# Kernel optimization log

Hardware: AMD Instinct MI355X
Metric: run time of the kernel (lower is better)

The kernel has to match this reference:

```python
import jax, jax.numpy as jnp
import numpy as np

CNN_DIM = 256
CLASS_NUM = 6
NHOPS = 2
ATT_DIM = 50


def conv1d(x, w, b, pad):
    # x: [B, Cin, L], w: [Cout, Cin, K]
    y = jax.lax.conv_general_dilated(x, w, (1,), [(pad, pad)],
                                     dimension_numbers=('NCH', 'OIH', 'NCH'))
    return y + b[None, :, None]


def setup_inputs() -> dict:
    key = jax.random.key(0)
    ks = jax.random.split(key, 16)
    B, L, V, GE, DE = 8, 128, 30000, 300, 100
    IN = GE + DE
    C = CLASS_NUM
    s = 0.02
    inp = {}
    inp['x'] = jax.random.randint(ks[0], (B, L), 0, V)
    inp['x_len'] = L  # python int, stands in for x_len[0] (max length)
    inp['x_mask'] = jnp.ones((B, L), dtype=jnp.float32)
    inp['gen_table'] = jax.random.normal(ks[1], (V, GE), jnp.float32) * s
    inp['domain_table'] = jax.random.normal(ks[2], (V, DE), jnp.float32) * s
    inp['w1'] = jax.random.normal(ks[3], (128, IN, 5)) * s
    inp['b1'] = jnp.zeros((128,))
    inp['w2'] = jax.random.normal(ks[4], (128, IN, 3)) * s
    inp['b2'] = jnp.zeros((128,))
    inp['w3'] = jax.random.normal(ks[5], (256, 256, 5)) * s
    inp['b3'] = jnp.zeros((256,))
    inp['w4'] = jax.random.normal(ks[6], (256, 256, 5)) * s
    inp['b4'] = jnp.zeros((256,))
    inp['w5'] = jax.random.normal(ks[7], (256, 256, 5)) * s
    inp['b5'] = jnp.zeros((256,))
    inp['wq'] = jax.random.normal(ks[8], (CNN_DIM, ATT_DIM)) * s
    inp['bq'] = jnp.zeros((ATT_DIM,))
    inp['wv'] = jax.random.normal(ks[9], (CNN_DIM, ATT_DIM)) * s
    inp['bv'] = jnp.zeros((ATT_DIM,))
    inp['vv'] = jax.random.normal(ks[10], (ATT_DIM,)) * s
    inp['wf'] = jax.random.normal(ks[11], (2 * CNN_DIM + 3 * C, 2 * CNN_DIM)) * s
    inp['bf'] = jnp.zeros((2 * CNN_DIM,))
    inp['wc'] = jax.random.normal(ks[12], (2 * CNN_DIM, C)) * s
    inp['bc'] = jnp.zeros((C,))
    return inp


def reference(x, x_len, x_mask, gen_table, domain_table,
              w1, b1, w2, b2, w3, b3, w4, b4, w5, b5,
              wq, bq, wv, bv, vv, wf, bf, wc, bc):
    # embeddings (dropout omitted: eval mode)
    emb = jnp.concatenate([gen_table[x], domain_table[x]], axis=2)  # [B,L,400]
    xe = jnp.swapaxes(emb, 1, 2)  # [B,400,L]
    xc = jax.nn.relu(jnp.concatenate([conv1d(xe, w1, b1, 2),
                                      conv1d(xe, w2, b2, 1)], axis=1))
    xc = jax.nn.relu(conv1d(xc, w3, b3, 2))
    xc = jax.nn.relu(conv1d(xc, w4, b4, 2))
    xc = jax.nn.relu(conv1d(xc, w5, b5, 2))
    xc = jnp.swapaxes(xc, 1, 2)[:, :x_len, :]  # [B,L,256]
    mask = x_mask[:, :x_len]
    # perceptron (additive) self-attention: v^T tanh(Wq q_i + Wv v_j)
    q = xc @ wq + bq  # [B,L,50]
    v = xc @ wv + bv  # [B,L,50]
    scores = jnp.tanh(q[:, :, None, :] + v[:, None, :, :]) @ vv  # [B,L,L]
    scores = jnp.where(mask[:, None, :] == 0, -1e9, scores)
    attn = jax.nn.softmax(scores, axis=2)
    merged = jnp.einsum('bij,bjd->bid', attn, xc) * mask[:, :, None]
    xc = xc + merged
    B, L, D = xc.shape
    # grid features: (i,j) -> [h_i, h_j]
    features = jnp.concatenate([
        jnp.broadcast_to(xc[:, :, None, :], (B, L, L, D)),
        jnp.broadcast_to(xc[:, None, :, :], (B, L, L, D))], axis=3)  # [B,L,L,512]
    # upper-triangular validity mask on the grid
    m2 = jnp.triu(mask[:, None, :] * mask[:, :, None])[..., None]  # [B,L,L,1]
    logits = features @ wc + bc  # [B,L,L,C]
    for _ in range(NHOPS):
        probs = logits
        lg = probs * m2
        lm = jnp.maximum(jnp.max(lg, axis=1), jnp.max(lg, axis=2))  # [B,L,C]
        row = jnp.broadcast_to(lm[:, :, None, :], (B, L, L, lm.shape[-1]))
        grid = jnp.concatenate([row, jnp.swapaxes(row, 1, 2)], axis=3)  # [B,L,L,2C]
        features = jnp.concatenate([features, grid, probs], axis=3) @ wf + bf
        logits = features @ wc + bc
    return logits
```

## Files before the change

### kernel.cpp

```cpp
#include <hip/hip_runtime.h>
#include <math.h>

#define LSEQ 128
#define BB 8
#define M_TOK (BB*LSEQ)

typedef __attribute__((ext_vector_type(8))) short short8;
typedef __attribute__((ext_vector_type(4))) float floatx4;

__device__ __forceinline__ unsigned short bf16_rne(float v) {
    union { float f; unsigned u; } a; a.f = v;
    return (unsigned short)((a.u + 0x7fffu + ((a.u >> 16) & 1u)) >> 16);
}
__device__ __forceinline__ float bf16_to_f(unsigned short h) {
    union { unsigned u; float f; } b; b.u = ((unsigned)h) << 16;
    return b.f;
}
__device__ __forceinline__ void split2(float v, unsigned short& h, unsigned short& l) {
    h = bf16_rne(v);
    l = bf16_rne(v - bf16_to_f(h));
}

struct PreArgs {
    const float *w1, *w2, *w3, *w4, *w5;
    unsigned short *B1h, *B1l, *B2h, *B2l, *B3h, *B3l, *B4h, *B4l, *B5h, *B5l;
    const int* x;
    const float* gen;
    const float* dom;
    unsigned short *Eh, *El;
    const float* wf;
    const float* wc;
    float* Wfc;
};
__global__ __launch_bounds__(256) void stage_kernel(PreArgs a) {
    int y = blockIdx.y;
    int tid = threadIdx.x;
    if (y < 3) {
        const float* w = (y == 0) ? a.w3 : (y == 1) ? a.w4 : a.w5;
        unsigned short* dh = (y == 0) ? a.B3h : (y == 1) ? a.B4h : a.B5h;
        unsigned short* dl = (y == 0) ? a.B3l : (y == 1) ? a.B4l : a.B5l;
        int idx = blockIdx.x * 256 + tid;
        int j = idx & 7;
        int n = (idx >> 3) & 255;
        int g = idx >> 11;
        int cg = g & 31, kk = g >> 5;
        int ci = cg * 8 + j;
        float v = w[(n * 256 + ci) * 5 + kk];
        unsigned short h, l; split2(v, h, l);
        dh[idx] = h; dl[idx] = l;
    } else if (y == 3) {
        int idx = blockIdx.x * 256 + tid;
        if (idx >= 5 * 52 * 128 * 8) return;
        int j = idx & 7;
        int n = (idx >> 3) & 127;
        int g = idx >> 10;
        int cg = g % 52, kk = g / 52;
        int ci = cg * 8 + j;
        float v = (ci < 400) ? a.w1[(n * 400 + ci) * 5 + kk] : 0.f;
        unsigned short h, l; split2(v, h, l);
        a.B1h[idx] = h; a.B1l[idx] = l;
    } else if (y == 4) {
        int idx = blockIdx.x * 256 + tid;
        if (idx >= 3 * 52 * 128 * 8) return;
        int j = idx & 7;
        int n = (idx >> 3) & 127;
        int g = idx >> 10;
        int cg = g % 52, kk = g / 52;
        int ci = cg * 8 + j;
        float v = (ci < 400) ? a.w2[(n * 400 + ci) * 3 + kk] : 0.f;
        unsigned short h, l; split2(v, h, l);
        a.B2h[idx] = h; a.B2l[idx] = l;
    } else if (y == 5) {
        int m = blockIdx.x;
        if (m >= M_TOK) return;
        int t = a.x[m];
        for (int c = tid; c < 416; c += 256) {
            float v = (c < 300) ? a.gen[t * 300 + c]
                    : (c < 400) ? a.dom[t * 100 + (c - 300)] : 0.f;
            unsigned short h, l; split2(v, h, l);
            a.Eh[m * 416 + c] = h;
            a.El[m * 416 + c] = l;
        }
    } else {
        int r = blockIdx.x;
        if (r >= 512 || tid >= 64) return;
        int l = tid;
        float p[6] = {0,0,0,0,0,0};
        const float* row = a.wf + r * 512;
        #pragma unroll
        for (int k = 0; k < 8; ++k) {
            int n = l + 64 * k;
            float v = row[n];
            #pragma unroll
            for (int c = 0; c < 6; ++c) p[c] += v * a.wc[n * 6 + c];
        }
        #pragma unroll
        for (int c = 0; c < 6; ++c)
            for (int off = 32; off >= 1; off >>= 1) p[c] += __shfl_xor(p[c], off, 64);
        if (l == 0) {
            #pragma unroll
            for (int c = 0; c < 6; ++c) a.Wfc[r * 6 + c] = p[c];
        }
    }
}

__global__ __launch_bounds__(256) void conv1_mfma(
        const unsigned short* __restrict__ Eh, const unsigned short* __restrict__ El,
        const unsigned short* __restrict__ B1h, const unsigned short* __restrict__ B1l,
        const unsigned short* __restrict__ B2h, const unsigned short* __restrict__ B2l,
        const float* __restrict__ b1, const float* __restrict__ b2,
        unsigned short* __restrict__ Xoh, unsigned short* __restrict__ Xol,
        const float* __restrict__ wf, const float* __restrict__ bf,
        const float* __restrict__ wc, const float* __restrict__ Wfc,
        float* __restrict__ U) {
    __shared__ __align__(16) unsigned short xsh[20 * 424];
    __shared__ __align__(16) unsigned short xsl[20 * 424];
    int by = blockIdx.y;
    int tid = threadIdx.x;
    if (by == 4) {
        if (tid >= 64) return;
        int l = tid;
        for (int i = 0; i < 9; ++i) {
            int r = blockIdx.x + 64 * i;
            if (r >= 531) break;
            const float* row = (r < 530) ? (wf + r * 512) : bf;
            float p[12];
            #pragma unroll
            for (int c = 0; c < 12; ++c) p[c] = 0.f;
            #pragma unroll
            for (int k = 0; k < 8; ++k) {
                int n = l + 64 * k;
                float v = row[n];
                #pragma unroll
                for (int c = 0; c < 6; ++c) {
                    p[c]     += v * wc[n * 6 + c];
                    p[c + 6] += v * Wfc[n * 6 + c];
                }
            }
            #pragma unroll
            for (int c = 0; c < 12; ++c)
                for (int off = 32; off >= 1; off >>= 1) p[c] += __shfl_xor(p[c], off, 64);
            if (l == 0) {
                #pragma unroll
                for (int c = 0; c < 12; ++c) U[r * 12 + c] = p[c];
            }
        }
        return;
    }
    int mt = blockIdx.x;
    int p0 = mt * 16;
    int b = p0 >> 7, l0 = p0 & 127;
    for (int i = tid; i < 2 * 1040; i += 256) {
        int sel = i >= 1040;
        int u2 = sel ? i - 1040 : i;
        int j = u2 / 52, cg = u2 % 52;
        int l = l0 - 2 + j;
        short8 v = {0,0,0,0,0,0,0,0};
        if (l >= 0 && l < 128) {
            const unsigned short* src = (sel ? El : Eh) + (b * 128 + l) * 416 + cg * 8;
            v = *(const short8*)src;
        }
        *(short8*)((sel ? xsl : xsh) + j * 424 + cg * 8) = v;
    }
    __syncthreads();
    int w = tid >> 6, lane = tid & 63;
    int m = lane & 15, q = lane >> 4;
    bool br2 = (by >= 2);
    int n0b = (by & 1) * 64;
    int nB = n0b + w * 16 + m;
    floatx4 acc0 = {0,0,0,0}, acc1 = {0,0,0,0}, acc2 = {0,0,0,0};
    if (!br2) {
        for (int kk = 0; kk < 5; ++kk) {
            const unsigned short* arh = xsh + (m + kk) * 424;
            const unsigned short* arl = xsl + (m + kk) * 424;
            #pragma unroll
            for (int u = 0; u < 13; ++u) {
                short8 ah = *(const short8*)(arh + u * 32 + q * 8);
                short8 al = *(const short8*)(arl + u * 32 + q * 8);
                int boff = (((kk * 52 + u * 4 + q) * 128) + nB) * 8;
                short8 bh = *(const short8*)(B1h + boff);
                short8 bl = *(const short8*)(B1l + boff);
                acc0 = __builtin_amdgcn_mfma_f32_16x16x32_bf16(ah, bh, acc0, 0, 0, 0);
                acc1 = __builtin_amdgcn_mfma_f32_16x16x32_bf16(ah, bl, acc1, 0, 0, 0);
                acc2 = __builtin_amdgcn_mfma_f32_16x16x32_bf16(al, bh, acc2, 0, 0, 0);
            }
        }
    } else {
        for (int kk = 0; kk < 3; ++kk) {
            const unsigned short* arh = xsh + (m + kk + 1) * 424;
            const unsigned short* arl = xsl + (m + kk + 1) * 424;
            #pragma unroll
            for (int u = 0; u < 13; ++u) {
                short8 ah = *(const short8*)(arh + u * 32 + q * 8);
                short8 al = *(const short8*)(arl + u * 32 + q * 8);
                int boff = (((kk * 52 + u * 4 + q) * 128) + nB) * 8;
                short8 bh = *(const short8*)(B2h + boff);
                short8 bl = *(const short8*)(B2l + boff);
                acc0 = __builtin_amdgcn_mfma_f32_16x16x32_bf16(ah, bh, acc0, 0, 0, 0);
                acc1 = __builtin_amdgcn_mfma_f32_16x16x32_bf16(ah, bl, acc1, 0, 0, 0);
                acc2 = __builtin_amdgcn_mfma_f32_16x16x32_bf16(al, bh, acc2, 0, 0, 0);
            }
        }
    }
    __syncthreads();
    float* fl = (float*)xsh;
    #pragma unroll
    for (int reg = 0; reg < 4; ++reg)
        fl[(q * 4 + reg) * 68 + w * 16 + m] = acc0[reg] + acc1[reg] + acc2[reg];
    __syncthreads();
    int ocb = br2 ? 128 + n0b : n0b;
    const float* bias = br2 ? b2 : b1;
    #pragma unroll
    for (int i = 0; i < 4; ++i) {
        int e = tid + 256 * i;
        int mm = e >> 6, nn = e & 63;
        float val = fl[mm * 68 + nn] + bias[n0b + nn];
        val = fmaxf(val, 0.f);
        unsigned short h, l; split2(val, h, l);
        int o = (p0 + mm) * 256 + ocb + nn;
        Xoh[o] = h; Xol[o] = l;
    }
}

__global__ __launch_bounds__(256) void conv256_mfma(
        const unsigned short* __restrict__ Xih, const unsigned short* __restrict__ Xil,
        const unsigned short* __restrict__ Bh, const unsigned short* __restrict__ Bl,
        const float* __restrict__ bias, int outmode,
        unsigned short* __restrict__ Xoh, unsigned short* __restrict__ Xol,
        float* __restrict__ fout) {
    __shared__ __align__(16) unsigned short xsh[20 * 264];
    __shared__ __align__(16) unsigned short xsl[20 * 264];
    int mt = blockIdx.x;
    int p0 = mt * 16;
    int b = p0 >> 7, l0 = p0 & 127;
    int n0 = blockIdx.y * 64;
    int tid = threadIdx.x;
    for (int i = tid; i < 2 * 640; i += 256) {
        int sel = i >= 640;
        int u2 = sel ? i - 640 : i;
        int j = u2 >> 5, cg = u2 & 31;
        int l = l0 - 2 + j;
        short8 v = {0,0,0,0,0,0,0,0};
        if (l >= 0 && l < 128) {
            const unsigned short* src = (sel ? Xil : Xih) + (b * 128 + l) * 256 + cg * 8;
            v = *(const short8*)src;
        }
        *(short8*)((sel ? xsl : xsh) + j * 264 + cg * 8) = v;
    }
    __syncthreads();
    int w = tid >> 6, lane = tid & 63;
    int m = lane & 15, q = lane >> 4;
    int nB = n0 + w * 16 + m;
    floatx4 acc0 = {0,0,0,0}, acc1 = {0,0,0,0}, acc2 = {0,0,0,0};
    for (int kk = 0; kk < 5; ++kk) {
        const unsigned short* arh = xsh + (m + kk) * 264;
        const unsigned short* arl = xsl + (m + kk) * 264;
        #pragma unroll
        for (int u = 0; u < 8; ++u) {
            short8 ah = *(const short8*)(arh + u * 32 + q * 8);
            short8 al = *(const short8*)(arl + u * 32 + q * 8);
            int boff = (((kk * 32 + u * 4 + q) * 256) + nB) * 8;
            short8 bh = *(const short8*)(Bh + boff);
            short8 bl = *(const short8*)(Bl + boff);
            acc0 = __builtin_amdgcn_mfma_f32_16x16x32_bf16(ah, bh, acc0, 0, 0, 0);
        acc1 = __builtin_amdgcn_mfma_f32_16x16x32_bf16(ah, bl, acc1, 0, 0, 0);
            acc2 = __builtin_amdgcn_mfma_f32_16x16x32_bf16(al, bh, acc2, 0, 0, 0);
        }
    }
    __syncthreads();
    float* fl = (float*)xsh;
    #pragma unroll
    for (int reg = 0; reg < 4; ++reg)
        fl[(q * 4 + reg) * 68 + w * 16 + m] = acc0[reg] + acc1[reg] + acc2[reg];
    __syncthreads();
    #pragma unroll
    for (int i = 0; i < 4; ++i) {
        int e = tid + 256 * i;
        int mm = e >> 6, nn = e & 63;
        float val = fl[mm * 68 + nn] + bias[n0 + nn];
        val = fmaxf(val, 0.f);
        int o = (p0 + mm) * 256 + n0 + nn;
        if (outmode == 0) {
            unsigned short h, l; split2(val, h, l);
            Xoh[o] = h; Xol[o] = l;
        } else {
            fout[o] = val;
        }
    }
}

__global__ __launch_bounds__(128) void qv_v2(const float* __restrict__ xc,
        const float* __restrict__ wq, const float* __restrict__ bq,
        const float* __restrict__ wv, const float* __restrict__ bv,
        float* __restrict__ q, float* __restrict__ v) {
    int m = blockIdx.x;
    int tid = threadIdx.x;
    int w = tid >> 6, d = tid & 63;
    if (d >= 50) return;
    const float* W = w ? wv : wq;
    float a = w ? bv[d] : bq[d];
    const float* xm = xc + m * 256;
    #pragma unroll 8
    for (int c = 0; c < 256; ++c) a += xm[c] * W[c * 50 + d];
    (w ? v : q)[m * 50 + d] = a;
}

__global__ __launch_bounds__(256) void attn_v2(const float* __restrict__ xc,
        const float* __restrict__ q, const float* __restrict__ v,
        const float* __restrict__ vv, const float* __restrict__ xmask,
        const float* __restrict__ wc, const float* __restrict__ bc,
        float* __restrict__ xc2, float* __restrict__ f0, float* __restrict__ g0) {
    __shared__ float vs[128 * 50];
    __shared__ float spart[128], aarr[128], xrow[256], qrow[52], vvs[52], red[4];
    int bi = blockIdx.x;
    int b = bi >> 7;
    int tid = threadIdx.x;
    for (int idx = tid; idx < 128 * 50; idx += 256) vs[idx] = v[b * 6400 + idx];
    if (tid < 50) { qrow[tid] = q[bi * 50 + tid]; vvs[tid] = vv[tid]; }
    __syncthreads();
    int j = tid & 127, half = tid >> 7;
    int d0 = half * 25;
    const float* vj = vs + j * 50 + d0;
    float s = 0.f;
    #pragma unroll
    for (int d = 0; d < 25; ++d) {
        float x = qrow[d0 + d] + vj[d];
        float e = __expf(2.f * x);
        s += (1.f - 2.f / (e + 1.f)) * vvs[d0 + d];
    }
    if (half) spart[j] = s;
    __syncthreads();
    float stot = 0.f;
    if (!half) {
        stot = s + spart[j];
        if (xmask[b * LSEQ + j] == 0.f) stot = -1e9f;
    }
    if (tid < 128) {
        float m = stot;
        #pragma unroll
        for (int off = 32; off >= 1; off >>= 1) m = fmaxf(m, __shfl_xor(m, off, 64));
        if ((tid & 63) == 0) red[tid >> 6] = m;
    }
    __syncthreads();
    float mx = fmaxf(red[0], red[1]);
    float e = 0.f;
    if (tid < 128) {
        e = __expf(stot - mx);
        float su = e;
        #pragma unroll
        for (int off = 32; off >= 1; off >>= 1) su += __shfl_xor(su, off, 64);
        if ((tid & 63) == 0) red[2 + (tid >> 6)] = su;
    }
    __syncthreads();
    float denom = red[2] + red[3];
    if (tid < 128) aarr[j] = e / denom;
    __syncthreads();
    float maskI = xmask[bi];
    const float* xcb = xc + b * LSEQ * 256;
    float acc = 0.f;
    #pragma unroll 8
    for (int jj = 0; jj < 128; ++jj) acc += aarr[jj] * xcb[jj * 256 + tid];
    float val = xc[bi * 256 + tid] + acc * maskI;
    xc2[bi * 256 + tid] = val;
    xrow[tid] = val;
    __syncthreads();
    int grp = tid >> 4, l16 = tid & 15;
    if (grp < 12) {
        int c = grp % 6, gsel = grp / 6;
        const float* wcc = wc + gsel * 256 * 6 + c;
        float a = 0.f;
        #pragma unroll
        for (int ch = l16; ch < 256; ch += 16) a += xrow[ch] * wcc[ch * 6];
        #pragma unroll
        for (int off = 8; off >= 1; off >>= 1) a += __shfl_down(a, off, 16);
        if (l16 == 0) {
            if (gsel == 0) f0[bi * 6 + c] = a + bc[c];
            else           g0[bi * 6 + c] = a;
        }
    }
}

__global__ __launch_bounds__(128) void lm_scan_v3(const float* __restrict__ f,
        const float* __restrict__ g, int stride, float* __restrict__ lm) {
    __shared__ float sf[128], sg[128];
    int bc = blockIdx.x;
    int b = bc / 6, c = bc - b * 6;
    int p = threadIdx.x;
    float fv = f[(b * LSEQ + p) * stride + c];
    float gv = g[(b * LSEQ + p) * stride + c];
    sf[p] = fv; sg[p] = gv;
    __syncthreads();
    float pf = fv, sgx = gv;
    #pragma unroll
    for (int off = 1; off < 128; off <<= 1) {
        float a = (p >= off) ? sf[p - off] : -INFINITY;
        float d = (p + off < 128) ? sg[p + off] : -INFINITY;
        __syncthreads();
        pf = fmaxf(pf, a); sgx = fmaxf(sgx, d);
        sf[p] = pf; sg[p] = sgx;
        __syncthreads();
    }
    float M1 = pf + gv;
    if (p < LSEQ - 1) M1 = fmaxf(M1, 0.f);
    float M2 = fv + sgx;
    if (p > 0) M2 = fmaxf(M2, 0.f);
    lm[(b * LSEQ + p) * 6 + c] = fmaxf(M1, M2);
}

__global__ __launch_bounds__(64) void hopfold_kernel(const float* __restrict__ xc2,
        const float* __restrict__ U, const float* __restrict__ lm0,
        const float* __restrict__ f0, const float* __restrict__ g0,
        const float* __restrict__ bc,
        float* __restrict__ outF, float* __restrict__ outG) {
    int m = blockIdx.x;
    int y = blockIdx.y;
    int tid = threadIdx.x;
    const float* Urows = U + (y ? 256 : 0) * 12;
    float p[12];
    #pragma unroll
    for (int c = 0; c < 12; ++c) p[c] = 0.f;
    for (int k = tid; k < 256; k += 64) {
        float a = xc2[m * 256 + k];
        const float* ur = Urows + k * 12;
        #pragma unroll
        for (int c = 0; c < 12; ++c) p[c] += a * ur[c];
    }
    #pragma unroll
    for (int c = 0; c < 12; ++c)
        for (int off = 32; off >= 1; off >>= 1) p[c] += __shfl_xor(p[c], off, 64);
    if (tid == 0) {
        const float* Bb = U + (y ? 518 : 512) * 12;
        const float* Db = U + 524 * 12;
        const float* fg = y ? g0 : f0;
        float* out = y ? outG : outF;
        float lmv[6], fgv[6];
        #pragma unroll
        for (int j = 0; j < 6; ++j) { lmv[j] = lm0[m * 6 + j]; fgv[j] = fg[m * 6 + j]; }
        #pragma unroll
        for (int c = 0; c < 12; ++c) {
            float s = p[c];
            #pragma unroll
            for (int j = 0; j < 6; ++j) s += lmv[j] * Bb[j * 12 + c] + fgv[j] * Db[j * 12 + c];
            if (!y) { s += U[530 * 12 + c]; if (c < 6) s += bc[c]; }
            out[m * 12 + c] = s;
        }
    }
}

__global__ __launch_bounds__(128) void f2g2_kernel(const float* __restrict__ f1phi,
        const float* __restrict__ g1gam, const float* __restrict__ lm1,
        const float* __restrict__ U, const float* __restrict__ bc,
        float* __restrict__ f2, float* __restrict__ g2) {
    __shared__ float Us[19 * 12], bcs[6];
    int tid = threadIdx.x;
    for (int i = tid; i < 19 * 12; i += 128) Us[i] = U[512 * 12 + i];
    if (tid < 6) bcs[tid] = bc[tid];
    __syncthreads();
    int m = blockIdx.x * 128 + tid;
    float lmv[6], f1v[6], g1v[6];
    #pragma unroll
    for (int j = 0; j < 6; ++j) {
        lmv[j] = lm1[m * 6 + j];
        f1v[j] = f1phi[m * 12 + j];
        g1v[j] = g1gam[m * 12 + j];
    }
    #pragma unroll
    for (int c = 0; c < 6; ++c) {
        float sf = f1phi[m * 12 + 6 + c] + Us[18 * 12 + c] + bcs[c];
        float sg = g1gam[m * 12 + 6 + c];
        #pragma unroll
        for (int j = 0; j < 6; ++j) {
            sf += lmv[j] * Us[j * 12 + c]       + f1v[j] * Us[(12 + j) * 12 + c];
            sg += lmv[j] * Us[(6 + j) * 12 + c] + g1v[j] * Us[(12 + j) * 12 + c];
        }
        f2[m * 6 + c] = sf;
        g2[m * 6 + c] = sg;
    }
}

__global__ __launch_bounds__(256) void writeout_kernel(const float* __restrict__ f2,
        const float* __restrict__ g2, float* __restrict__ out) {
    int idx = blockIdx.x * 256 + threadIdx.x;
    int c = idx % 6;
    int r = idx / 6;
    int j = r & 127;
    int bi = r >> 7;
    int b = bi >> 7;
    out[idx] = f2[bi * 6 + c] + g2[(b * LSEQ + j) * 6 + c];
}

extern "C" void kernel_launch(void* const* d_in, const int* in_sizes, int n_in,
                              void* d_out, int out_size, void* d_ws, size_t ws_size,
                              hipStream_t stream) {
    const int*   x     = (const int*)d_in[0];
    const float* xmask = (const float*)d_in[2];
    const float* gen   = (const float*)d_in[3];
    const float* dom   = (const float*)d_in[4];
    const float* w1    = (const float*)d_in[5];
    const float* b1    = (const float*)d_in[6];
    const float* w2    = (const float*)d_in[7];
    const float* b2    = (const float*)d_in[8];
    const float* w3    = (const float*)d_in[9];
    const float* b3    = (const float*)d_in[10];
    const float* w4    = (const float*)d_in[11];
    const float* b4    = (const float*)d_in[12];
    const float* w5    = (const float*)d_in[13];
    const float* b5    = (const float*)d_in[14];
    const float* wq    = (const float*)d_in[15];
    const float* bq    = (const float*)d_in[16];
    const float* wv    = (const float*)d_in[17];
    const float* bv    = (const float*)d_in[18];
    const float* vv    = (const float*)d_in[19];
    const float* wf    = (const float*)d_in[20];
    const float* bf    = (const float*)d_in[21];
    const float* wc    = (const float*)d_in[22];
    const float* bc    = (const float*)d_in[23];

    float* fb = (float*)d_ws;
    float* bufB  = fb;
    float* xc2   = bufB  + 262144;
    float* qb    = xc2   + 262144;
    float* vb    = qb    + 51200;
    float* Wfc   = vb    + 51200;
    float* U     = Wfc   + 3072;
    float* f0    = U     + 6376;
    float* g0    = f0    + 6144;
    float* lm0   = g0    + 6144;
    float* lm1   = lm0   + 6144;
    float* f1phi = lm1   + 6144;
    float* g1gam = f1phi + 12288;
    float* f2    = g1gam + 12288;
    float* g2    = f2    + 6144;
    unsigned short* sb = (unsigned short*)(g2 + 6144 + 32);
    unsigned short* Eh  = sb;             sb += 425984;
    unsigned short* El  = sb;             sb += 425984;
    unsigned short* B1h = sb;             sb += 266240;
    unsigned short* B1l = sb;             sb += 266240;
    unsigned short* B2h = sb;             sb += 159744;
    unsigned short* B2l = sb;             sb += 159744;
    unsigned short* B3h = sb;             sb += 327680;
    unsigned short* B3l = sb;             sb += 327680;
    unsigned short* B4h = sb;             sb += 327680;
    unsigned short* B4l = sb;             sb += 327680;
    unsigned short* B5h = sb;             sb += 327680;
    unsigned short* B5l = sb;             sb += 327680;
    unsigned short* X3h = sb;             sb += 262144;
    unsigned short* X3l = sb;             sb += 262144;
    unsigned short* X4h = sb;             sb += 262144;
    unsigned short* X4l = sb;             sb += 262144;

    PreArgs pa;
    pa.w1 = w1; pa.w2 = w2; pa.w3 = w3; pa.w4 = w4; pa.w5 = w5;
    pa.B1h = B1h; pa.B1l = B1l; pa.B2h = B2h; pa.B2l = B2l;
    pa.B3h = B3h; pa.B3l = B3l; pa.B4h = B4h; pa.B4l = B4l;
    pa.B5h = B5h; pa.B5l = B5l;
    pa.x = x; pa.gen = gen; pa.dom = dom; pa.Eh = Eh; pa.El = El;
    pa.wf = wf; pa.wc = wc; pa.Wfc = Wfc;
    stage_kernel<<<dim3(1280, 7), 256, 0, stream>>>(pa);

    conv1_mfma<<<dim3(64, 5), 256, 0, stream>>>(Eh, El, B1h, B1l, B2h, B2l, b1, b2,
                                                X3h, X3l, wf, bf, wc, Wfc, U);
    conv256_mfma<<<dim3(64, 4), 256, 0, stream>>>(X3h, X3l, B3h, B3l, b3, 0,
                                                  X4h, X4l, nullptr);
    conv256_mfma<<<dim3(64, 4), 256, 0, stream>>>(X4h, X4l, B4h, B4l, b4, 0,
                                                  X3h, X3l, nullptr);
    conv256_mfma<<<dim3(64, 4), 256, 0, stream>>>(X3h, X3l, B5h, B5l, b5, 1,
                                                  nullptr, nullptr, bufB);

    qv_v2<<<M_TOK, 128, 0, stream>>>(bufB, wq, bq, wv, bv, qb, vb);
    attn_v2<<<M_TOK, 256, 0, stream>>>(bufB, qb, vb, vv, xmask, wc, bc, xc2, f0, g0);

    lm_scan_v3<<<48, 128, 0, stream>>>(f0, g0, 6, lm0);
    hopfold_kernel<<<dim3(M_TOK, 2), 64, 0, stream>>>(xc2, U, lm0, f0, g0, bc, f1phi, g1gam);
    lm_scan_v3<<<48, 128, 0, stream>>>(f1phi, g1gam, 12, lm1);
    f2g2_kernel<<<8, 128, 0, stream>>>(f1phi, g1gam, lm1, U, bc, f2, g2);

    writeout_kernel<<<(BB*LSEQ*LSEQ*6)/256, 256, 0, stream>>>(f2, g2, (float*)d_out);
}
```

Before: 241.0 us.

## Fuse lm max-scans into hop kernels and merge final tail into one kernel

Removes the two separate lm_scan launches by computing the prefix and suffix maxima inside hopfold (a wave-wide masked reduction per token) and inside a new tail kernel (a warp shuffle scan over a shared-memory transposed tile). The f2/g2 computation and the full-grid writeout are merged into tail2_kernel, so the intermediate f2/g2 buffers are no longer written and re-read. This cuts the launch count from five to two and drops the small serial kernels. In exchange, every block redundantly recomputes the per-batch scans and reloads the per-batch f/g data.

```diff
diff --git a/kernel.cpp b/kernel.cpp
--- a/kernel.cpp
+++ b/kernel.cpp
@@ -263,7 +263,7 @@
             short8 bh = *(const short8*)(Bh + boff);
             short8 bl = *(const short8*)(Bl + boff);
             acc0 = __builtin_amdgcn_mfma_f32_16x16x32_bf16(ah, bh, acc0, 0, 0, 0);
-        acc1 = __builtin_amdgcn_mfma_f32_16x16x32_bf16(ah, bl, acc1, 0, 0, 0);
+            acc1 = __builtin_amdgcn_mfma_f32_16x16x32_bf16(ah, bl, acc1, 0, 0, 0);
             acc2 = __builtin_amdgcn_mfma_f32_16x16x32_bf16(al, bh, acc2, 0, 0, 0);
         }
     }
@@ -380,65 +380,68 @@
     }
 }
 
-__global__ __launch_bounds__(128) void lm_scan_v3(const float* __restrict__ f,
-        const float* __restrict__ g, int stride, float* __restrict__ lm) {
-    __shared__ float sf[128], sg[128];
-    int bc = blockIdx.x;
-    int b = bc / 6, c = bc - b * 6;
-    int p = threadIdx.x;
-    float fv = f[(b * LSEQ + p) * stride + c];
-    float gv = g[(b * LSEQ + p) * stride + c];
-    sf[p] = fv; sg[p] = gv;
-    __syncthreads();
-    float pf = fv, sgx = gv;
-    #pragma unroll
-    for (int off = 1; off < 128; off <<= 1) {
-        float a = (p >= off) ? sf[p - off] : -INFINITY;
-        float d = (p + off < 128) ? sg[p + off] : -INFINITY;
-        __syncthreads();
-        pf = fmaxf(pf, a); sgx = fmaxf(sgx, d);
-        sf[p] = pf; sg[p] = sgx;
-        __syncthreads();
-    }
-    float M1 = pf + gv;
-    if (p < LSEQ - 1) M1 = fmaxf(M1, 0.f);
-    float M2 = fv + sgx;
-    if (p > 0) M2 = fmaxf(M2, 0.f);
-    lm[(b * LSEQ + p) * 6 + c] = fmaxf(M1, M2);
-}
-
-__global__ __launch_bounds__(64) void hopfold_kernel(const float* __restrict__ xc2,
-        const float* __restrict__ U, const float* __restrict__ lm0,
-        const float* __restrict__ f0, const float* __restrict__ g0,
-        const float* __restrict__ bc,
+__global__ __launch_bounds__(64) void hopfold_v2(const float* __restrict__ xc2,
+        const float* __restrict__ U, const float* __restrict__ f0,
+        const float* __restrict__ g0, const float* __restrict__ bc,
         float* __restrict__ outF, float* __restrict__ outG) {
     int m = blockIdx.x;
     int y = blockIdx.y;
     int tid = threadIdx.x;
+    int b = m >> 7, t = m & 127;
+    const float* fbp = f0 + b * 768;
+    const float* gbp = g0 + b * 768;
+    float pf[6], sgm[6];
+    #pragma unroll
+    for (int c = 0; c < 6; ++c) { pf[c] = -INFINITY; sgm[c] = -INFINITY; }
+    #pragma unroll
+    for (int r = 0; r < 2; ++r) {
+        int p = tid + 64 * r;
+        bool fok = (p <= t), gok = (p >= t);
+        #pragma unroll
+        for (int c = 0; c < 6; ++c) {
+            float fv = fbp[p * 6 + c];
+            float gv = gbp[p * 6 + c];
+            pf[c]  = fmaxf(pf[c],  fok ? fv : -INFINITY);
+            sgm[c] = fmaxf(sgm[c], gok ? gv : -INFINITY);
+        }
+    }
+    #pragma unroll
+    for (int c = 0; c < 6; ++c) {
+        #pragma unroll
+        for (int off = 32; off >= 1; off >>= 1) {
+            pf[c]  = fmaxf(pf[c],  __shfl_xor(pf[c],  off, 64));
+            sgm[c] = fmaxf(sgm[c], __shfl_xor(sgm[c], off, 64));
+        }
+    }
     const float* Urows = U + (y ? 256 : 0) * 12;
-    float p[12];
-    #pragma unroll
-    for (int c = 0; c < 12; ++c) p[c] = 0.f;
+    float acc[12];
+    #pragma unroll
+    for (int c = 0; c < 12; ++c) acc[c] = 0.f;
     for (int k = tid; k < 256; k += 64) {
         float a = xc2[m * 256 + k];
         const float* ur = Urows + k * 12;
         #pragma unroll
-        for (int c = 0; c < 12; ++c) p[c] += a * ur[c];
+        for (int c = 0; c < 12; ++c) acc[c] += a * ur[c];
     }
     #pragma unroll
     for (int c = 0; c < 12; ++c)
-        for (int off = 32; off >= 1; off >>= 1) p[c] += __shfl_xor(p[c], off, 64);
+        for (int off = 32; off >= 1; off >>= 1) acc[c] += __shfl_xor(acc[c], off, 64);
     if (tid == 0) {
         const float* Bb = U + (y ? 518 : 512) * 12;
         const float* Db = U + 524 * 12;
-        const float* fg = y ? g0 : f0;
         float* out = y ? outG : outF;
         float lmv[6], fgv[6];
         #pragma unroll
-        for (int j = 0; j < 6; ++j) { lmv[j] = lm0[m * 6 + j]; fgv[j] = fg[m * 6 + j]; }
+        for (int c = 0; c < 6; ++c) {
+            float fvt = fbp[t * 6 + c], gvt = gbp[t * 6 + c];
+            float M1 = pf[c] + gvt;  if (t < LSEQ - 1) M1 = fmaxf(M1, 0.f);
+            float M2 = fvt + sgm[c]; if (t > 0)        M2 = fmaxf(M2, 0.f);
+            lmv[c] = fmaxf(M1, M2);
+            fgv[c] = y ? gvt : fvt;
+        }
         #pragma unroll
         for (int c = 0; c < 12; ++c) {
-            float s = p[c];
+            float s = acc[c];
             #pragma unroll
             for (int j = 0; j < 6; ++j) s += lmv[j] * Bb[j * 12 + c] + fgv[j] * Db[j * 12 + c];
             if (!y) { s += U[530 * 12 + c]; if (c < 6) s += bc[c]; }
@@ -447,46 +450,83 @@
     }
 }
 
-__global__ __launch_bounds__(128) void f2g2_kernel(const float* __restrict__ f1phi,
-        const float* __restrict__ g1gam, const float* __restrict__ lm1,
-        const float* __restrict__ U, const float* __restrict__ bc,
-        float* __restrict__ f2, float* __restrict__ g2) {
-    __shared__ float Us[19 * 12], bcs[6];
+__global__ __launch_bounds__(128) void tail2_kernel(const float* __restrict__ f1phi,
+        const float* __restrict__ g1gam, const float* __restrict__ U,
+        const float* __restrict__ bc, float* __restrict__ out) {
+    __shared__ float fT[12 * 132], gT[12 * 132];
+    __shared__ float pmax[6 * 132], smax[6 * 132];
+    __shared__ float Ut[19 * 12], bcs[8];
+    int bi = blockIdx.x;
+    int b = bi >> 7, i = bi & 127;
     int tid = threadIdx.x;
-    for (int i = tid; i < 19 * 12; i += 128) Us[i] = U[512 * 12 + i];
+    for (int k = tid; k < 1536; k += 128) {
+        int p = k / 12, c = k - p * 12;
+        fT[c * 132 + p] = f1phi[b * 1536 + k];
+        gT[c * 132 + p] = g1gam[b * 1536 + k];
+    }
+    for (int k = tid; k < 228; k += 128) Ut[k] = U[512 * 12 + k];
     if (tid < 6) bcs[tid] = bc[tid];
     __syncthreads();
-    int m = blockIdx.x * 128 + tid;
-    float lmv[6], f1v[6], g1v[6];
-    #pragma unroll
-    for (int j = 0; j < 6; ++j) {
-        lmv[j] = lm1[m * 6 + j];
-        f1v[j] = f1phi[m * 12 + j];
-        g1v[j] = g1gam[m * 12 + j];
-    }
+    int w = tid >> 6, l = tid & 63;
+    if (w == 0) {
+        for (int c = 0; c < 6; ++c) {
+            float v0 = fT[c * 132 + 2 * l], v1 = fT[c * 132 + 2 * l + 1];
+            float sc = fmaxf(v0, v1);
+            #pragma unroll
+            for (int off = 1; off < 64; off <<= 1) {
+                float o = __shfl_up(sc, off, 64);
+                if (l >= off) sc = fmaxf(sc, o);
+            }
+            float E = __shfl_up(sc, 1, 64); if (l == 0) E = -INFINITY;
+            pmax[c * 132 + 2 * l] = fmaxf(E, v0);
+            pmax[c * 132 + 2 * l + 1] = sc;
+        }
+    } else {
+        for (int c = 0; c < 6; ++c) {
+            int i0 = 127 - 2 * l, i1 = 126 - 2 * l;
+            float v0 = gT[c * 132 + i0], v1 = gT[c * 132 + i1];
+            float sc = fmaxf(v0, v1);
+            #pragma unroll
+            for (int off = 1; off < 64; off <<= 1) {
+                float o = __shfl_up(sc, off, 64);
+                if (l >= off) sc = fmaxf(sc, o);
+            }
+            float E = __shfl_up(sc, 1, 64); if (l == 0) E = -INFINITY;
+            smax[c * 132 + i0] = fmaxf(E, v0);
+            smax[c * 132 + i1] = sc;
+        }
+    }
+    __syncthreads();
+    int j = tid;
+    float lmj[6], lmi[6];
     #pragma unroll
     for (int c = 0; c < 6; ++c) {
-        float sf = f1phi[m * 12 + 6 + c] + Us[18 * 12 + c] + bcs[c];
-        float sg = g1gam[m * 12 + 6 + c];
-        #pragma unroll
-        for (int j = 0; j < 6; ++j) {
-            sf += lmv[j] * Us[j * 12 + c]       + f1v[j] * Us[(12 + j) * 12 + c];
-            sg += lmv[j] * Us[(6 + j) * 12 + c] + g1v[j] * Us[(12 + j) * 12 + c];
-        }
-        f2[m * 6 + c] = sf;
-        g2[m * 6 + c] = sg;
-    }
-}
-
-__global__ __launch_bounds__(256) void writeout_kernel(const float* __restrict__ f2,
-        const float* __restrict__ g2, float* __restrict__ out) {
-    int idx = blockIdx.x * 256 + threadIdx.x;
-    int c = idx % 6;
-    int r = idx / 6;
-    int j = r & 127;
-    int bi = r >> 7;
-    int b = bi >> 7;
-    out[idx] = f2[bi * 6 + c] + g2[(b * LSEQ + j) * 6 + c];
+        float M1 = pmax[c * 132 + j] + gT[c * 132 + j];
+        if (j < LSEQ - 1) M1 = fmaxf(M1, 0.f);
+        float M2 = fT[c * 132 + j] + smax[c * 132 + j];
+        if (j > 0) M2 = fmaxf(M2, 0.f);
+        lmj[c] = fmaxf(M1, M2);
+        float N1 = pmax[c * 132 + i] + gT[c * 132 + i];
+        if (i < LSEQ - 1) N1 = fmaxf(N1, 0.f);
+        float N2 = fT[c * 132 + i] + smax[c * 132 + i];
+        if (i > 0) N2 = fmaxf(N2, 0.f);
+        lmi[c] = fmaxf(N1, N2);
+    }
+    float res[6];
+    #pragma unroll
+    for (int c = 0; c < 6; ++c) {
+        float sf = fT[(6 + c) * 132 + i] + Ut[18 * 12 + c] + bcs[c];
+        float sg = gT[(6 + c) * 132 + j];
+        #pragma unroll
+        for (int jj = 0; jj < 6; ++jj) {
+            sf += lmi[jj] * Ut[jj * 12 + c]       + fT[jj * 132 + i] * Ut[(12 + jj) * 12 + c];
+            sg += lmj[jj] * Ut[(6 + jj) * 12 + c] + gT[jj * 132 + j] * Ut[(12 + jj) * 12 + c];
+        }
+        res[c] = sf + sg;
+    }
+    float* op = out + (size_t)bi * 768 + j * 6;
+    #pragma unroll
+    for (int c = 0; c < 6; ++c) op[c] = res[c];
 }
 
 extern "C" void kernel_launch(void* const* d_in, const int* in_sizes, int n_in,
@@ -525,13 +565,9 @@
     float* U     = Wfc   + 3072;
     float* f0    = U     + 6376;
     float* g0    = f0    + 6144;
-    float* lm0   = g0    + 6144;
-    float* lm1   = lm0   + 6144;
-    float* f1phi = lm1   + 6144;
+    float* f1phi = g0    + 6144;
     float* g1gam = f1phi + 12288;
-    float* f2    = g1gam + 12288;
-    float* g2    = f2    + 6144;
-    unsigned short* sb = (unsigned short*)(g2 + 6144 + 32);
+    unsigned short* sb = (unsigned short*)(g1gam + 12288 + 32);
     unsigned short* Eh  = sb;             sb += 425984;
     unsigned short* El  = sb;             sb += 425984;
     unsigned short* B1h = sb;             sb += 266240;
@@ -570,10 +606,6 @@
     qv_v2<<<M_TOK, 128, 0, stream>>>(bufB, wq, bq, wv, bv, qb, vb);
     attn_v2<<<M_TOK, 256, 0, stream>>>(bufB, qb, vb, vv, xmask, wc, bc, xc2, f0, g0);
 
-    lm_scan_v3<<<48, 128, 0, stream>>>(f0, g0, 6, lm0);
-    hopfold_kernel<<<dim3(M_TOK, 2), 64, 0, stream>>>(xc2, U, lm0, f0, g0, bc, f1phi, g1gam);
-    lm_scan_v3<<<48, 128, 0, stream>>>(f1phi, g1gam, 12, lm1);
-    f2g2_kernel<<<8, 128, 0, stream>>>(f1phi, g1gam, lm1, U, bc, f2, g2);
-
-    writeout_kernel<<<(BB*LSEQ*LSEQ*6)/256, 256, 0, stream>>>(f2, g2, (float*)d_out);
-}
+    hopfold_v2<<<dim3(M_TOK, 2), 64, 0, stream>>>(xc2, U, f0, g0, bc, f1phi, g1gam);
+    tail2_kernel<<<M_TOK, 128, 0, stream>>>(f1phi, g1gam, U, bc, (float*)d_out);
+}
```

After: 241.2 us. About the same (+0.1%).
